# Kernel optimization log

Hardware: AMD Instinct MI355X
Metric: run time of the kernel (lower is better)

The kernel has to match this reference:

```python
import jax, jax.numpy as jnp
import numpy as np

B, T, C, D = 4, 2048, 48, 512
L = 16                    # transcript length per video (distinct labels)
K = 9                     # bdy_kernel
CS = 15                   # cs_kernel
N_TR = L - 1
N_CAND = 3 * N_TR         # candidate_mul * pt_num
WIN_LEN = int(T / L * 0.15)   # int(t / t_len * win_scale)
ALPHA, BETA, GAMMA, TEMP = 1.0, 1.0, 0.1, 0.1
LOG2 = float(np.log(2.0))

def _bdy_kernel():
    ker = np.zeros((K, K), np.float32)
    c = K // 2
    ker[:c, :c] = 1; ker[c:, c:] = 1
    ker[:c, c:] = -1; ker[c:, :c] = -1
    ker[c, c] = 0
    return jnp.asarray(ker)

BDY_KER = _bdy_kernel()

def bdy_score_fn(prob):
    # prob: [T, C]; sliding windows of size K over time (zero padded)
    c = K // 2
    pad = jnp.pad(prob, ((c, c), (0, 0)))
    win = pad[jnp.arange(T)[:, None] + jnp.arange(K)[None, :]]       # [T,K,C]
    p = win[:, :, None, :]                                           # [T,K,1,C]
    m = (p + win[:, None, :, :]) / 2                                 # [T,K,K,C]
    # torch F.kl_div((m+1e-32).log(), p) = p*(log p - log(m+1e-32)), xlogy(0)=0
    kl = jnp.sum(jnp.where(p > 0, p * (jnp.log(jnp.where(p > 0, p, 1.0)) - jnp.log(m + 1e-32)), 0.0), -1)
    js = (kl + jnp.swapaxes(kl, 1, 2)) / 2
    js = -(js / LOG2 * 2 - 1)                                        # [T,K,K]
    return jnp.mean(BDY_KER[None] * js, axis=(-1, -2))               # [T]

def dp(cls_score):
    # cls_score: [N_TR, N_CAND]; min-cost alignment DP, inner jj-loop vectorized
    cost = -cls_score
    n_tr, n_x = N_TR, N_CAND
    W = 2 * n_tr + 1
    col = jnp.arange(W)
    inf = jnp.float32(jnp.inf)
    tr_at = jnp.clip(col // 2, 0, n_tr - 1)
    even = (col % 2 == 0)
    ge2 = col >= 2

    def init_cols(ii):
        c0 = jnp.where(ii < n_x - n_tr, 0.0, inf)
        c1 = jnp.where(ii <= n_x - n_tr, cost[0, ii], inf)
        d1 = jnp.where(ii <= n_x - n_tr, 1, 0).astype(jnp.int32)
        return c0, c1, d1

    c0, c1, d1 = init_cols(0)
    row0 = jnp.full((W,), inf).at[0].set(c0).at[1].set(c1)
    dir0 = jnp.zeros((W,), jnp.int32).at[1].set(d1)

    def step(prev, ii):
        dm1 = jnp.concatenate([jnp.full((1,), inf), prev[:-1]])
        dm2 = jnp.concatenate([jnp.full((2,), inf), prev[:-2]])
        c_at = cost[:, ii][tr_at]
        even_val = jnp.minimum(prev, dm1)
        even_dir = jnp.where(prev < dm1, 0, 1).astype(jnp.int32)
        odd_val = c_at + jnp.minimum(dm1, dm2)
        odd_dir = jnp.where(dm1 < dm2, 1, 2).astype(jnp.int32)
        c0, c1, d1 = init_cols(ii)
        new = jnp.where(ge2, jnp.where(even, even_val, odd_val), inf)
        new = new.at[0].set(c0).at[1].set(c1)
        dirs = jnp.where(ge2, jnp.where(even, even_dir, odd_dir), 0).astype(jnp.int32)
        dirs = dirs.at[1].set(d1)
        return new, dirs

    last, dirs = jax.lax.scan(step, row0, jnp.arange(1, n_x))
    dir_mat = jnp.concatenate([dir0[None], dirs], 0)                 # [n_x, W]
    cur_j0 = jnp.where(last[2 * n_tr] < last[2 * n_tr - 1], 2 * n_tr, 2 * n_tr - 1).astype(jnp.int32)

    def bt(cur_j, x):
        ii, dir_row = x
        is_odd = (cur_j % 2) == 1
        out_idx = jnp.where(is_odd, cur_j // 2, jnp.int32(n_tr))     # n_tr = OOB -> dropped
        new_j = cur_j - dir_row[cur_j]
        return new_j, (out_idx, ii.astype(jnp.int32))

    _, (oi, ovals) = jax.lax.scan(bt, cur_j0, (jnp.arange(n_x), dir_mat), reverse=True)
    return jnp.zeros((n_tr,), jnp.int32).at[oi].set(ovals, mode='drop')

def detect(logit, tr):
    # logit: [T,C] (detached), tr: [L] ints -> boundary frame indices [N_TR]
    prob = jax.nn.softmax(logit, -1)
    score = bdy_score_fn(prob).at[0].set(-jnp.inf)
    backup = score
    pos = jnp.arange(T)

    def pick(s, _):
        i = jnp.argmax(s)
        return jnp.where(jnp.abs(pos - i) <= WIN_LEN, -jnp.inf, s), i

    _, cand = jax.lax.scan(pick, score, None, length=N_CAND)
    cand = jnp.sort(cand)                                            # [N_CAND]
    # class-transition score at candidate points
    cc = CS // 2
    pairs = jnp.pad(prob[:, tr], ((cc, cc), (0, 0)))                 # [T+2cc, L]
    win = pairs[cand[:, None] + jnp.arange(CS)[None, :]]             # [N_CAND, CS, L]
    first, second = win[:, :, :-1], win[:, :, 1:]
    k0 = jnp.where(jnp.arange(CS) < cc, 1.0, -1.0)[None, :, None]
    cls = jnp.sum(k0 * (first - second), axis=1) / (2 * CS)          # [N_CAND, N_TR]
    cls = cls.T + backup[cand][None, :]                              # [N_TR, N_CAND]
    return cand[dp(cls)]

def _forward(tok_logit, fr_logit, vid_multi_hot, feat, mask, transcript):
    y = vid_multi_hot
    tok_loss = jnp.mean(-(y * jax.nn.log_sigmoid(tok_logit) + (1 - y) * jax.nn.log_sigmoid(-tok_logit)))
    # boundary detection on detached logits
    bdy = jax.vmap(detect)(jax.lax.stop_gradient(fr_logit), transcript)   # [B, N_TR]
    pse = jax.vmap(lambda b, tr: tr[jnp.sum(jnp.arange(T)[:, None] >= b[None, :], axis=1)])(bdy, transcript)
    # frame CE (bgw==1.0 path, full mask so no -100 labels)
    logp = jax.nn.log_softmax(fr_logit, -1)
    ce = -jnp.take_along_axis(logp, pse[..., None], axis=-1)[..., 0]
    m = mask.astype(ce.dtype)
    fr_loss = jnp.sum(ce * m) / jnp.sum(m)
    # global-local contrast
    tok_feat = jax.lax.stop_gradient(feat[:, :C, :])
    fr_feat = feat[:, C:, :]

    def glc_one(tok, fr, pse_i, tr, m_i):
        labels = jnp.sort(tr)                                        # = unique(pse[mask]), distinct labels
        oh = (pse_i[None, :] == labels[:, None]).astype(fr.dtype) * m_i[None, :]
        cnt = jnp.maximum(jnp.sum(oh, 1, keepdims=True), 1.0)
        la = (oh @ fr) / cnt
        la = la / jnp.maximum(jnp.linalg.norm(la, axis=-1, keepdims=True), 1e-12)
        tk = tok / jnp.maximum(jnp.linalg.norm(tok, axis=-1, keepdims=True), 1e-12)
        sim = (la @ tk.T) / TEMP                                     # [L, C]
        return jnp.mean(-jnp.take_along_axis(jax.nn.log_softmax(sim, -1), labels[:, None], axis=-1))

    glc_loss = jnp.mean(jax.vmap(glc_one)(tok_feat, fr_feat, pse, transcript, mask.astype(feat.dtype)))
    return ALPHA * tok_loss + BETA * fr_loss + GAMMA * glc_loss

def setup_inputs() -> dict:
    key = jax.random.key(0)
    ks = jax.random.split(key, 5)
    tok_logit = jax.random.normal(ks[0], (B, C), jnp.float32)
    fr_logit = jax.random.normal(ks[1], (B, T, C), jnp.float32)
    mask = jnp.ones((B, T), bool)
    transcript = jax.vmap(lambda k: jax.random.permutation(k, C)[:L])(jax.random.split(ks[2], B)).astype(jnp.int32)
    vid_multi_hot = jax.random.uniform(ks[3], (B, C), jnp.float32)
    feat = jax.random.normal(ks[4], (B, C + T, D), jnp.float32)
    return {"epoch": 5, "tok_logit": tok_logit, "fr_logit": fr_logit, "mask": mask,
            "transcript": transcript, "vid_multi_hot": vid_multi_hot, "feat": feat}

def reference(epoch, tok_logit, fr_logit, mask, transcript, vid_multi_hot, feat):
    # epoch >= warm_epc (=0), so the full loss path runs
    return _forward(tok_logit, fr_logit, vid_multi_hot, feat, mask, transcript)
```

## Files before the change

### kernel.cpp

```cpp
#include <hip/hip_runtime.h>
#include <math.h>

#define BB 4
#define TT 2048
#define CC 48
#define DD 512
#define LL 16
#define NTR 15
#define NCAND 45
#define WINLEN 19
#define CSW 15
#define CCHALF 7

static __device__ __forceinline__ float wave_reduce_sum(float v) {
    for (int off = 32; off; off >>= 1) v += __shfl_down(v, off);
    return v;
}

#define DPPMAX(x, ctrl) fmaxf((x), __int_as_float(__builtin_amdgcn_update_dpp( \
    __float_as_int(x), __float_as_int(x), (ctrl), 0xF, 0xF, false)))

__global__ __launch_bounds__(256) void k_lse(const float* __restrict__ fr,
                                             float* __restrict__ lse) {
    int row = blockIdx.x * 4 + (threadIdx.x >> 6);
    int lane = threadIdx.x & 63;
    float xv = (lane < CC) ? fr[(size_t)row * CC + lane] : -INFINITY;
    float m = xv;
    for (int off = 32; off; off >>= 1) m = fmaxf(m, __shfl_down(m, off));
    m = __shfl(m, 0);
    float e = (lane < CC) ? __expf(xv - m) : 0.f;
    float s = wave_reduce_sum(e);
    if (lane == 0) lse[row] = m + __logf(s);
}

__global__ __launch_bounds__(64) void k_score(const float* __restrict__ fr,
                                              const float* __restrict__ lse,
                                              float* __restrict__ score) {
    int row = blockIdx.x;
    int b = row / TT, t = row % TT;
    __shared__ float sp[9][CC];
    __shared__ float slp[9][CC];
    __shared__ float lse_s[9];
    int tid = threadIdx.x;
    if (tid < 9) {
        int r = t - 4 + tid;
        lse_s[tid] = (r >= 0 && r < TT) ? lse[b * TT + r] : 0.f;
    }
    __syncthreads();
    for (int idx = tid; idx < 9 * CC; idx += 64) {
        int i = idx / CC, c = idx - (idx / CC) * CC;
        int r = t - 4 + i;
        float pv = 0.f, lv = 0.f;
        if (r >= 0 && r < TT) {
            float x = fr[((size_t)b * TT + r) * CC + c];
            lv = x - lse_s[i];
            pv = __expf(lv);
        }
        sp[i][c] = pv;
        slp[i][c] = lv;
    }
    __syncthreads();
    float acc = 0.f;
    for (int idx = tid; idx < 4 * CC; idx += 64) {
        int i = idx / CC, c = idx - (idx / CC) * CC;
        acc += -2.f * sp[i][c] * slp[i][c];
    }
    for (int item = tid; item < 36 * CC; item += 64) {
        int pidx = item / CC, c = item - pidx * CC;
        int i = 0, rem = pidx;
        while (rem >= 8 - i) { rem -= 8 - i; ++i; }
        int j = i + 1 + rem;
        float wgt = ((i < 4) == (j < 4)) ? 1.f : -1.f;
        float pi = sp[i][c], pj = sp[j][c];
        float logm = __logf(0.5f * (pi + pj) + 1e-32f);
        acc -= wgt * (pi + pj) * logm;
    }
    acc = wave_reduce_sum(acc);
    if (tid == 0) {
        const float SC = -2.0f / (81.0f * 0.6931471805599453f);
        score[row] = (t == 0) ? -INFINITY : SC * acc;
    }
}

__global__ __launch_bounds__(64) void k_pick(const float* __restrict__ score,
                                             int* __restrict__ cand,
                                             float* __restrict__ backup) {
    int b = blockIdx.x;
    int lane = threadIdx.x;
    __shared__ float s[64 * 33];
    __shared__ int cl[NCAND];
    for (int t = lane; t < TT; t += 64) s[t + (t >> 5)] = score[(size_t)b * TT + t];
    __syncthreads();
    float v[32];
    #pragma unroll
    for (int k = 0; k < 32; ++k) v[k] = s[lane * 33 + k];
    int base = lane << 5;
    for (int it = 0; it < NCAND; ++it) {
        float best = -INFINITY; int bi = 0;
        #pragma unroll
        for (int k = 31; k >= 0; --k)
            if (v[k] >= best) { best = v[k]; bi = k; }
        float m = best;
        m = DPPMAX(m, 0x111); m = DPPMAX(m, 0x112);
        m = DPPMAX(m, 0x114); m = DPPMAX(m, 0x118);
        m = DPPMAX(m, 0x142); m = DPPMAX(m, 0x143);
        float gmax = __int_as_float(__builtin_amdgcn_readlane(__float_as_int(m), 63));
        unsigned long long ball = __ballot(best == gmax);
        int sl = (int)(__ffsll((long long)ball) - 1);
        int mp = __builtin_amdgcn_readlane(base + bi, sl);
        if (lane == 0) cl[it] = mp;
        int llo = mp - WINLEN - base;
        int lhi = mp + WINLEN - base;
        unsigned lowm = (llo <= 0) ? 0xffffffffu : ((llo >= 32) ? 0u : ~((1u << llo) - 1u));
        unsigned him  = (lhi >= 31) ? 0xffffffffu : ((lhi < 0) ? 0u : ((2u << lhi) - 1u));
        unsigned wm = lowm & him;
        #pragma unroll
        for (int k = 0; k < 32; ++k)
            if (wm & (1u << k)) v[k] = -INFINITY;
    }
    __syncthreads();
    if (lane < NCAND) {
        int my = cl[lane];
        int rank = 0;
        for (int i = 0; i < NCAND; ++i) rank += (cl[i] < my) ? 1 : 0;
        cand[b * 64 + rank] = my;
        backup[b * 64 + rank] = s[my + (my >> 5)];
    }
}

__global__ __launch_bounds__(256) void k_dp(const float* __restrict__ fr,
                                            const float* __restrict__ lse,
                                            const int* __restrict__ cand,
                                            const float* __restrict__ backup,
                                            const int* __restrict__ transcript,
                                            int* __restrict__ labels_out,
                                            int* __restrict__ rowmap,
                                            float* __restrict__ fr_part,
                                            float* __restrict__ la) {
    int b = blockIdx.x;
    __shared__ float cost[NTR][NCAND];
    __shared__ int tr_s[LL];
    __shared__ int cand_s[NCAND];
    __shared__ float backup_s[NCAND];
    __shared__ signed char dir_mat[NCAND][32];
    __shared__ int bdy_s[NTR];
    __shared__ int rank_s[LL];
    __shared__ float redf[4];
    int tid = threadIdx.x;
    int wave = tid >> 6, lane = tid & 63;
    if (tid < LL) tr_s[tid] = transcript[b * LL + tid];
    if (tid < NCAND) {
        cand_s[tid] = cand[b * 64 + tid];
        backup_s[tid] = backup[b * 64 + tid];
    }

    {
        float4 z = {0.f, 0.f, 0.f, 0.f};
        float4* lz = (float4*)(la + (size_t)b * LL * DD);
        #pragma unroll
        for (int i = 0; i < LL * DD / 4 / 256; ++i) lz[i * 256 + tid] = z;
    }
    __syncthreads();

    for (int e = tid; e < NTR * NCAND; e += 256) {
        int j = e / NCAND, ii = e - (e / NCAND) * NCAND;
        int cpos = cand_s[ii];
        int trj = tr_s[j], trj1 = tr_s[j + 1];
        float sum = 0.f;
        #pragma unroll
        for (int k = 0; k < CSW; ++k) {
            int r = cpos - CCHALF + k;
            float a = 0.f, d2 = 0.f;
            if (r >= 0 && r < TT) {
                size_t ro = (size_t)b * TT + r;
                float ls = lse[ro];
                a  = __expf(fr[ro * CC + trj]  - ls);
                d2 = __expf(fr[ro * CC + trj1] - ls);
            }
            sum += ((k < CCHALF) ? 1.f : -1.f) * (a - d2);
        }
        cost[j][ii] = -(sum / 30.f + backup_s[ii]);
    }
    __syncthreads();

    if (tid < 64) {
        float prev = INFINITY;
        if (tid == 0) prev = 0.f;
        if (tid == 1) prev = cost[0][0];
        if (tid < 31) dir_mat[0][tid] = (tid == 1) ? (signed char)1 : (signed char)0;
        for (int ii = 1; ii < NCAND; ++ii) {
            float dm1 = __shfl_up(prev, 1); if (tid < 1) dm1 = INFINITY;
            float dm2 = __shfl_up(prev, 2); if (tid < 2) dm2 = INFINITY;
            int trat = tid >> 1; if (trat > NTR - 1) trat = NTR - 1;
            float c_at = cost[trat][ii];
            float ev = fminf(prev, dm1);
            int ed = (prev < dm1) ? 0 : 1;
            float ov = c_at + fminf(dm1, dm2);
            int od = (dm1 < dm2) ? 1 : 2;
            float nv; int nd;
            if (tid >= 2) {
                if ((tid & 1) == 0) { nv = ev; nd = ed; }
                else { nv = ov; nd = od; }
            } else { nv = INFINITY; nd = 0; }
            if (tid == 0) { nv = (ii < NCAND - NTR) ? 0.f : INFINITY; nd = 0; }
            if (tid == 1) {
                nv = (ii <= NCAND - NTR) ? cost[0][ii] : INFINITY;
                nd = (ii <= NCAND - NTR) ? 1 : 0;
            }
            prev = nv;
            if (tid < 31) dir_mat[ii][tid] = (signed char)nd;
        }
        float v29 = __shfl(prev, 29);
        float v30 = __shfl(prev, 30);
        if (tid == 0) {
            int cur = (v30 < v29) ? 30 : 29;
            for (int ii = NCAND - 1; ii >= 0; --ii) {
                if (cur & 1) bdy_s[cur >> 1] = cand_s[ii];
                cur -= (int)dir_mat[ii][cur];
            }
        }
    }
    __syncthreads();

    if (tid < LL) {
        int myv = tr_s[tid];
        int r2 = 0;
        #pragma unroll
        for (int l2 = 0; l2 < LL; ++l2) r2 += (tr_s[l2] < myv) ? 1 : 0;
        rank_s[tid] = r2;
        labels_out[b * LL + r2] = myv;
    }
    __syncthreads();

    float facc = 0.f;
    for (int t = tid; t < TT; t += 256) {
        int cnt = 0;
        #pragma unroll
        for (int j = 0; j < NTR; ++j) cnt += (t >= bdy_s[j]) ? 1 : 0;
        int pv = tr_s[cnt];
        rowmap[b * TT + t] = rank_s[cnt];
        size_t ro = (size_t)b * TT + t;
        facc += lse[ro] - fr[ro * CC + pv];
    }
    facc = wave_reduce_sum(facc);
    if (lane == 0) redf[wave] = facc;
    __syncthreads();
    if (tid == 0) fr_part[b] = redf[0] + redf[1] + redf[2] + redf[3];
}

__global__ __launch_bounds__(256) void k_la(const float* __restrict__ feat,
                                            const int* __restrict__ rowmap,
                                            float* __restrict__ la) {
    int b = blockIdx.y;
    int t0 = blockIdx.x * 32;
    int tid = threadIdx.x;
    const float* frf = feat + ((size_t)b * (CC + TT) + CC) * DD;
    __shared__ int rm[32];
    if (tid < 32) rm[tid] = rowmap[b * TT + t0 + tid];
    __syncthreads();
    float ax = 0.f, ay = 0.f;
    int cur = rm[0];
    for (int k = 0; k < 32; ++k) {
        int r = rm[k];
        if (r != cur) {
            float* dst = la + ((size_t)b * LL + cur) * DD + tid * 2;
            atomicAdd(dst, ax);
            atomicAdd(dst + 1, ay);
            ax = 0.f; ay = 0.f; cur = r;
        }
        const float2* p = (const float2*)(frf + (size_t)(t0 + k) * DD);
        float2 v = p[tid];
        ax += v.x; ay += v.y;
    }
    float* dst = la + ((size_t)b * LL + cur) * DD + tid * 2;
    atomicAdd(dst, ax);
    atomicAdd(dst + 1, ay);
}

__global__ __launch_bounds__(256) void k_glc(const float* __restrict__ feat,
                                             const float* __restrict__ la,
                                             float* __restrict__ dots,
                                             float* __restrict__ ntk) {
    int c = blockIdx.x, b = blockIdx.y;
    __shared__ float tok_s[DD];
    __shared__ float redv[4];
    int tid = threadIdx.x;
    int wave = tid >> 6, lane = tid & 63;
    const float* tr = feat + ((size_t)b * (CC + TT) + c) * DD;
    float2 tv = ((const float2*)tr)[tid];
    ((float2*)tok_s)[tid] = tv;
    float vv = tv.x * tv.x + tv.y * tv.y;
    vv = wave_reduce_sum(vv);
    if (lane == 0) redv[wave] = vv;
    __syncthreads();
    if (tid == 0)
        ntk[b * CC + c] = fmaxf(sqrtf(redv[0] + redv[1] + redv[2] + redv[3]), 1e-12f);
    for (int l = wave; l < LL; l += 4) {
        const float4* lar = (const float4*)(la + ((size_t)b * LL + l) * DD);
        const float4* ts = (const float4*)tok_s;
        float dot = 0.f;
        #pragma unroll
        for (int jj = 0; jj < 2; ++jj) {
            int j = lane + jj * 64;
            float4 a = lar[j]; float4 w = ts[j];
            dot += a.x * w.x + a.y * w.y + a.z * w.z + a.w * w.w;
        }
        dot = wave_reduce_sum(dot);
        if (lane == 0) dots[((size_t)b * LL + l) * CC + c] = dot;
    }
}

__global__ __launch_bounds__(64) void k_term(const float* __restrict__ la,
                                             const float* __restrict__ dots,
                                             const float* __restrict__ ntk,
                                             const int* __restrict__ labels,
                                             float* __restrict__ terms) {
    int l = blockIdx.x, b = blockIdx.y;
    int lane = threadIdx.x;
    const float4* lar = (const float4*)(la + ((size_t)b * LL + l) * DD);
    float ss = 0.f;
    #pragma unroll
    for (int jj = 0; jj < 2; ++jj) {
        float4 a = lar[lane + jj * 64];
        ss += a.x * a.x + a.y * a.y + a.z * a.z + a.w * a.w;
    }
    ss = wave_reduce_sum(ss);
    float nla = fmaxf(sqrtf(__shfl(ss, 0)), 1e-12f);
    float sim = -INFINITY;
    if (lane < CC)
        sim = dots[((size_t)b * LL + l) * CC + lane] * 10.0f / (nla * ntk[b * CC + lane]);
    float mx = sim;
    for (int off = 32; off; off >>= 1) mx = fmaxf(mx, __shfl_down(mx, off));
    mx = __shfl(mx, 0);
    float e = (lane < CC) ? expf(sim - mx) : 0.f;
    float se = wave_reduce_sum(e);
    se = __shfl(se, 0);
    int lab = labels[b * LL + l];
    float sim_lab = __shfl(sim, lab);
    if (lane == 0) terms[b * LL + l] = (mx + logf(se)) - sim_lab;
}

__global__ __launch_bounds__(256) void k_combine(const float* __restrict__ tok_logit,
                                                 const float* __restrict__ vid,
                                                 const float* __restrict__ fr_part,
                                                 const float* __restrict__ terms,
                                                 float* __restrict__ out) {
    int tid = threadIdx.x;
    __shared__ float red[4];
    __shared__ float gterm;
    float acc = 0.f;
    if (tid < BB * CC) {
        float x = tok_logit[tid], y = vid[tid];
        float lsp = fminf(x, 0.f) - log1pf(expf(-fabsf(x)));
        float lsn = fminf(-x, 0.f) - log1pf(expf(-fabsf(x)));
        acc = -(y * lsp + (1.f - y) * lsn);
    }
    float w = wave_reduce_sum(acc);
    if ((tid & 63) == 0) red[tid >> 6] = w;
    if (tid < 64) {
        float g = terms[tid];
        g = wave_reduce_sum(g);
        if (tid == 0) gterm = g;
    }
    __syncthreads();
    if (tid == 0) {
        float s_tok = (red[0] + red[1] + red[2] + red[3]) / (float)(BB * CC);
        float sfr = fr_part[0] + fr_part[1] + fr_part[2] + fr_part[3];
        float s_fr = sfr / (float)(BB * TT);
        float glc = gterm / (float)(BB * LL);
        out[0] = s_tok + s_fr + 0.1f * glc;
    }
}

extern "C" void kernel_launch(void* const* d_in, const int* in_sizes, int n_in,
                              void* d_out, int out_size, void* d_ws, size_t ws_size,
                              hipStream_t stream) {
    (void)in_sizes; (void)n_in; (void)out_size; (void)ws_size;
    const float* tok_logit  = (const float*)d_in[1];
    const float* fr_logit   = (const float*)d_in[2];
    const int*   transcript = (const int*)d_in[4];
    const float* vid        = (const float*)d_in[5];
    const float* feat       = (const float*)d_in[6];

    char* ws = (char*)d_ws;
    float* lse     = (float*)(ws + 0);
    float* score   = (float*)(ws + 32768);
    float* la      = (float*)(ws + 65536);
    float* dots    = (float*)(ws + 196608);
    float* ntk     = (float*)(ws + 208896);
    float* terms   = (float*)(ws + 209664);
    float* fr_part = (float*)(ws + 209920);
    int*   labels  = (int*)(ws + 210176);
    int*   rowmap  = (int*)(ws + 210432);
    int*   cand    = (int*)(ws + 243200);
    float* backup  = (float*)(ws + 244224);
    float* out     = (float*)d_out;

    k_lse<<<BB * TT / 4, 256, 0, stream>>>(fr_logit, lse);
    k_score<<<BB * TT, 64, 0, stream>>>(fr_logit, lse, score);
    k_pick<<<BB, 64, 0, stream>>>(score, cand, backup);
    k_dp<<<BB, 256, 0, stream>>>(fr_logit, lse, cand, backup, transcript,
                                 labels, rowmap, fr_part, la);
    k_la<<<dim3(TT / 32, BB), 256, 0, stream>>>(feat, rowmap, la);
    k_glc<<<dim3(CC, BB), 256, 0, stream>>>(feat, la, dots, ntk);
    k_term<<<dim3(LL, BB), 64, 0, stream>>>(la, dots, ntk, labels, terms);
    k_combine<<<1, 256, 0, stream>>>(tok_logit, vid, fr_part, terms, out);
}
```

Measured before the change: 171.6 us.

## Fuse LSE into score kernel, merge term/combine, stage DP windows in LDS

Drops the separate log-sum-exp kernel: each k_score block now recomputes the LSE for its nine neighbouring rows and writes its own row's LSE for later kernels. k_term and k_combine are merged into one single-block k_final. k_pick loads scores straight from global memory with float4 reads instead of going through LDS. k_dp precomputes the candidate-window probabilities into LDS once rather than recomputing two exps per cost entry, and k_la switches to float4 loads split across two row halves. The aim is fewer launches and less redundant exp and memory work, at the cost of about nine times more LSE work in k_score and extra atomics in k_la.

```diff
diff --git a/kernel.cpp b/kernel.cpp
--- a/kernel.cpp
+++ b/kernel.cpp
@@ -20,21 +20,8 @@
 #define DPPMAX(x, ctrl) fmaxf((x), __int_as_float(__builtin_amdgcn_update_dpp( \
     __float_as_int(x), __float_as_int(x), (ctrl), 0xF, 0xF, false)))
 
-__global__ __launch_bounds__(256) void k_lse(const float* __restrict__ fr,
-                                             float* __restrict__ lse) {
-    int row = blockIdx.x * 4 + (threadIdx.x >> 6);
-    int lane = threadIdx.x & 63;
-    float xv = (lane < CC) ? fr[(size_t)row * CC + lane] : -INFINITY;
-    float m = xv;
-    for (int off = 32; off; off >>= 1) m = fmaxf(m, __shfl_down(m, off));
-    m = __shfl(m, 0);
-    float e = (lane < CC) ? __expf(xv - m) : 0.f;
-    float s = wave_reduce_sum(e);
-    if (lane == 0) lse[row] = m + __logf(s);
-}
-
 __global__ __launch_bounds__(64) void k_score(const float* __restrict__ fr,
-                                              const float* __restrict__ lse,
+                                              float* __restrict__ lse,
                                               float* __restrict__ score) {
     int row = blockIdx.x;
     int b = row / TT, t = row % TT;
@@ -42,22 +29,32 @@
     __shared__ float slp[9][CC];
     __shared__ float lse_s[9];
     int tid = threadIdx.x;
-    if (tid < 9) {
-        int r = t - 4 + tid;
-        lse_s[tid] = (r >= 0 && r < TT) ? lse[b * TT + r] : 0.f;
-    }
-    __syncthreads();
     for (int idx = tid; idx < 9 * CC; idx += 64) {
         int i = idx / CC, c = idx - (idx / CC) * CC;
         int r = t - 4 + i;
-        float pv = 0.f, lv = 0.f;
-        if (r >= 0 && r < TT) {
-            float x = fr[((size_t)b * TT + r) * CC + c];
-            lv = x - lse_s[i];
-            pv = __expf(lv);
-        }
+        sp[i][c] = (r >= 0 && r < TT) ? fr[((size_t)b * TT + r) * CC + c] : 0.f;
+    }
+    __syncthreads();
+    for (int i = 0; i < 9; ++i) {
+        int r = t - 4 + i;
+        bool valid = (r >= 0 && r < TT);
+        float xv = (tid < CC && valid) ? sp[i][tid] : -INFINITY;
+        float m = xv;
+        for (int off = 32; off; off >>= 1) m = fmaxf(m, __shfl_down(m, off));
+        m = __shfl(m, 0);
+        float e = (tid < CC && valid) ? __expf(xv - m) : 0.f;
+        float s = wave_reduce_sum(e);
+        if (tid == 0) lse_s[i] = valid ? (m + __logf(s)) : 0.f;
+    }
+    __syncthreads();
+    if (tid == 0) lse[row] = lse_s[4];
+    for (int idx = tid; idx < 9 * CC; idx += 64) {
+        int i = idx / CC, c = idx - (idx / CC) * CC;
+        int r = t - 4 + i;
+        float lv = 0.f, pv = 0.f;
+        if (r >= 0 && r < TT) { lv = sp[i][c] - lse_s[i]; pv = __expf(lv); }
+        slp[i][c] = lv;
         sp[i][c] = pv;
-        slp[i][c] = lv;
     }
     __syncthreads();
     float acc = 0.f;
@@ -87,13 +84,17 @@
                                              float* __restrict__ backup) {
     int b = blockIdx.x;
     int lane = threadIdx.x;
-    __shared__ float s[64 * 33];
     __shared__ int cl[NCAND];
-    for (int t = lane; t < TT; t += 64) s[t + (t >> 5)] = score[(size_t)b * TT + t];
-    __syncthreads();
     float v[32];
-    #pragma unroll
-    for (int k = 0; k < 32; ++k) v[k] = s[lane * 33 + k];
+    {
+        const float4* sp4 = (const float4*)(score + (size_t)b * TT + (lane << 5));
+        #pragma unroll
+        for (int q = 0; q < 8; ++q) {
+            float4 x = sp4[q];
+            v[q * 4 + 0] = x.x; v[q * 4 + 1] = x.y;
+            v[q * 4 + 2] = x.z; v[q * 4 + 3] = x.w;
+        }
+    }
     int base = lane << 5;
     for (int it = 0; it < NCAND; ++it) {
         float best = -INFINITY; int bi = 0;
@@ -124,7 +125,7 @@
         int rank = 0;
         for (int i = 0; i < NCAND; ++i) rank += (cl[i] < my) ? 1 : 0;
         cand[b * 64 + rank] = my;
-        backup[b * 64 + rank] = s[my + (my >> 5)];
+        backup[b * 64 + rank] = score[(size_t)b * TT + my];
     }
 }
 
@@ -138,6 +139,7 @@
                                             float* __restrict__ fr_part,
                                             float* __restrict__ la) {
     int b = blockIdx.x;
+    __shared__ float win[NCAND][CSW][LL + 1];
     __shared__ float cost[NTR][NCAND];
     __shared__ int tr_s[LL];
     __shared__ int cand_s[NCAND];
@@ -162,23 +164,27 @@
     }
     __syncthreads();
 
+    for (int e = tid; e < NCAND * CSW * LL; e += 256) {
+        int ii = e / (CSW * LL);
+        int rem = e - ii * (CSW * LL);
+        int k = rem >> 4;
+        int m = rem & 15;
+        int r = cand_s[ii] - CCHALF + k;
+        float p = 0.f;
+        if (r >= 0 && r < TT) {
+            size_t ro = (size_t)b * TT + r;
+            p = __expf(fr[ro * CC + tr_s[m]] - lse[ro]);
+        }
+        win[ii][k][m] = p;
+    }
+    __syncthreads();
+
     for (int e = tid; e < NTR * NCAND; e += 256) {
         int j = e / NCAND, ii = e - (e / NCAND) * NCAND;
-        int cpos = cand_s[ii];
-        int trj = tr_s[j], trj1 = tr_s[j + 1];
         float sum = 0.f;
         #pragma unroll
-        for (int k = 0; k < CSW; ++k) {
-            int r = cpos - CCHALF + k;
-            float a = 0.f, d2 = 0.f;
-            if (r >= 0 && r < TT) {
-                size_t ro = (size_t)b * TT + r;
-                float ls = lse[ro];
-                a  = __expf(fr[ro * CC + trj]  - ls);
-                d2 = __expf(fr[ro * CC + trj1] - ls);
-            }
-            sum += ((k < CCHALF) ? 1.f : -1.f) * (a - d2);
-        }
+        for (int k = 0; k < CSW; ++k)
+            sum += ((k < CCHALF) ? 1.f : -1.f) * (win[ii][k][j] - win[ii][k][j + 1]);
         cost[j][ii] = -(sum / 30.f + backup_s[ii]);
     }
     __syncthreads();
@@ -254,27 +260,29 @@
     int b = blockIdx.y;
     int t0 = blockIdx.x * 32;
     int tid = threadIdx.x;
+    int h = tid >> 7;
+    int col = tid & 127;
     const float* frf = feat + ((size_t)b * (CC + TT) + CC) * DD;
     __shared__ int rm[32];
     if (tid < 32) rm[tid] = rowmap[b * TT + t0 + tid];
     __syncthreads();
-    float ax = 0.f, ay = 0.f;
-    int cur = rm[0];
-    for (int k = 0; k < 32; ++k) {
+    float4 acc = {0.f, 0.f, 0.f, 0.f};
+    int cur = rm[h];
+    for (int k = h; k < 32; k += 2) {
         int r = rm[k];
         if (r != cur) {
-            float* dst = la + ((size_t)b * LL + cur) * DD + tid * 2;
-            atomicAdd(dst, ax);
-            atomicAdd(dst + 1, ay);
-            ax = 0.f; ay = 0.f; cur = r;
-        }
-        const float2* p = (const float2*)(frf + (size_t)(t0 + k) * DD);
-        float2 v = p[tid];
-        ax += v.x; ay += v.y;
-    }
-    float* dst = la + ((size_t)b * LL + cur) * DD + tid * 2;
-    atomicAdd(dst, ax);
-    atomicAdd(dst + 1, ay);
+            float* dst = la + ((size_t)b * LL + cur) * DD + col * 4;
+            atomicAdd(dst + 0, acc.x); atomicAdd(dst + 1, acc.y);
+            atomicAdd(dst + 2, acc.z); atomicAdd(dst + 3, acc.w);
+            acc.x = 0.f; acc.y = 0.f; acc.z = 0.f; acc.w = 0.f;
+            cur = r;
+        }
+        float4 v = ((const float4*)(frf + (size_t)(t0 + k) * DD))[col];
+        acc.x += v.x; acc.y += v.y; acc.z += v.z; acc.w += v.w;
+    }
+    float* dst = la + ((size_t)b * LL + cur) * DD + col * 4;
+    atomicAdd(dst + 0, acc.x); atomicAdd(dst + 1, acc.y);
+    atomicAdd(dst + 2, acc.z); atomicAdd(dst + 3, acc.w);
 }
 
 __global__ __launch_bounds__(256) void k_glc(const float* __restrict__ feat,
@@ -310,44 +318,44 @@
     }
 }
 
-__global__ __launch_bounds__(64) void k_term(const float* __restrict__ la,
-                                             const float* __restrict__ dots,
-                                             const float* __restrict__ ntk,
-                                             const int* __restrict__ labels,
-                                             float* __restrict__ terms) {
-    int l = blockIdx.x, b = blockIdx.y;
-    int lane = threadIdx.x;
-    const float4* lar = (const float4*)(la + ((size_t)b * LL + l) * DD);
-    float ss = 0.f;
-    #pragma unroll
-    for (int jj = 0; jj < 2; ++jj) {
-        float4 a = lar[lane + jj * 64];
-        ss += a.x * a.x + a.y * a.y + a.z * a.z + a.w * a.w;
-    }
-    ss = wave_reduce_sum(ss);
-    float nla = fmaxf(sqrtf(__shfl(ss, 0)), 1e-12f);
-    float sim = -INFINITY;
-    if (lane < CC)
-        sim = dots[((size_t)b * LL + l) * CC + lane] * 10.0f / (nla * ntk[b * CC + lane]);
-    float mx = sim;
-    for (int off = 32; off; off >>= 1) mx = fmaxf(mx, __shfl_down(mx, off));
-    mx = __shfl(mx, 0);
-    float e = (lane < CC) ? expf(sim - mx) : 0.f;
-    float se = wave_reduce_sum(e);
-    se = __shfl(se, 0);
-    int lab = labels[b * LL + l];
-    float sim_lab = __shfl(sim, lab);
-    if (lane == 0) terms[b * LL + l] = (mx + logf(se)) - sim_lab;
-}
-
-__global__ __launch_bounds__(256) void k_combine(const float* __restrict__ tok_logit,
-                                                 const float* __restrict__ vid,
-                                                 const float* __restrict__ fr_part,
-                                                 const float* __restrict__ terms,
-                                                 float* __restrict__ out) {
+__global__ __launch_bounds__(256) void k_final(const float* __restrict__ tok_logit,
+                                               const float* __restrict__ vid,
+                                               const float* __restrict__ fr_part,
+                                               const float* __restrict__ la,
+                                               const float* __restrict__ dots,
+                                               const float* __restrict__ ntk,
+                                               const int* __restrict__ labels,
+                                               float* __restrict__ out) {
     int tid = threadIdx.x;
+    int wave = tid >> 6, lane = tid & 63;
+    __shared__ float term_s[BB * LL];
     __shared__ float red[4];
     __shared__ float gterm;
+    for (int i = 0; i < 16; ++i) {
+        int job = wave * 16 + i;
+        int b = job >> 4;
+        const float4* lar = (const float4*)(la + (size_t)job * DD);
+        float ss = 0.f;
+        #pragma unroll
+        for (int jj = 0; jj < 2; ++jj) {
+            float4 a = lar[lane + jj * 64];
+            ss += a.x * a.x + a.y * a.y + a.z * a.z + a.w * a.w;
+        }
+        ss = wave_reduce_sum(ss);
+        float nla = fmaxf(sqrtf(__shfl(ss, 0)), 1e-12f);
+        float sim = -INFINITY;
+        if (lane < CC)
+            sim = dots[(size_t)job * CC + lane] * 10.0f / (nla * ntk[b * CC + lane]);
+        float mx = sim;
+        for (int off = 32; off; off >>= 1) mx = fmaxf(mx, __shfl_down(mx, off));
+        mx = __shfl(mx, 0);
+        float e = (lane < CC) ? expf(sim - mx) : 0.f;
+        float se = wave_reduce_sum(e);
+        se = __shfl(se, 0);
+        int lab = labels[job];
+        float sim_lab = __shfl(sim, lab);
+        if (lane == 0) term_s[job] = (mx + logf(se)) - sim_lab;
+    }
     float acc = 0.f;
     if (tid < BB * CC) {
         float x = tok_logit[tid], y = vid[tid];
@@ -356,9 +364,10 @@
         acc = -(y * lsp + (1.f - y) * lsn);
     }
     float w = wave_reduce_sum(acc);
-    if ((tid & 63) == 0) red[tid >> 6] = w;
+    if (lane == 0) red[wave] = w;
+    __syncthreads();
     if (tid < 64) {
-        float g = terms[tid];
+        float g = term_s[tid];
         g = wave_reduce_sum(g);
         if (tid == 0) gterm = g;
     }
@@ -388,7 +397,6 @@
     float* la      = (float*)(ws + 65536);
     float* dots    = (float*)(ws + 196608);
     float* ntk     = (float*)(ws + 208896);
-    float* terms   = (float*)(ws + 209664);
     float* fr_part = (float*)(ws + 209920);
     int*   labels  = (int*)(ws + 210176);
     int*   rowmap  = (int*)(ws + 210432);
@@ -396,13 +404,11 @@
     float* backup  = (float*)(ws + 244224);
     float* out     = (float*)d_out;
 
-    k_lse<<<BB * TT / 4, 256, 0, stream>>>(fr_logit, lse);
     k_score<<<BB * TT, 64, 0, stream>>>(fr_logit, lse, score);
     k_pick<<<BB, 64, 0, stream>>>(score, cand, backup);
     k_dp<<<BB, 256, 0, stream>>>(fr_logit, lse, cand, backup, transcript,
                                  labels, rowmap, fr_part, la);
     k_la<<<dim3(TT / 32, BB), 256, 0, stream>>>(feat, rowmap, la);
     k_glc<<<dim3(CC, BB), 256, 0, stream>>>(feat, la, dots, ntk);
-    k_term<<<dim3(LL, BB), 64, 0, stream>>>(la, dots, ntk, labels, terms);
-    k_combine<<<1, 256, 0, stream>>>(tok_logit, vid, fr_part, terms, out);
-}
+    k_final<<<1, 256, 0, stream>>>(tok_logit, vid, fr_part, la, dots, ntk, labels, out);
+}
```

New measurement: 203.7 us. 18.7% more time.
